# Performance work log

Measured on AMD Instinct MI355X. Metric: run time of the kernel, lower is better.

The kernel has to match this reference:

```python
import jax, jax.numpy as jnp
import numpy as np

FREQ_CUTOFF = 10.0
SAMPLING_RATE = 100.0
FILTER_TYPE = 'lowpass'

B, C, L = 64, 128, 8192


def setup_inputs() -> dict:
    key = jax.random.key(0)
    x = jax.random.normal(key, (B, C, L), dtype=jnp.float32)
    return {"x": x}


def reference(x):
    # x: [B, C, L]
    seq_len = x.shape[-1]
    x_fft = jnp.fft.fft(x, axis=-1)  # complex64 [B, C, L]
    freqs = jnp.fft.fftfreq(seq_len, 1.0 / SAMPLING_RATE)  # [L]
    if FILTER_TYPE == 'lowpass':
        mask = jnp.abs(freqs) < FREQ_CUTOFF
    elif FILTER_TYPE == 'highpass':
        mask = jnp.abs(freqs) > FREQ_CUTOFF
    else:
        raise ValueError('Invalid filter type: {}'.format(FILTER_TYPE))
    # Zero out masked frequency bins (faithful to original: lowpass zeroes |f| < cutoff)
    x_fft = jnp.where(mask[None, None, :], 0.0 + 0.0j, x_fft)
    x_filtered = jnp.real(jnp.fft.ifft(x_fft, axis=-1)).astype(jnp.float32)
    return x_filtered
```

## Files before the change

kernel.cpp:

```cpp
#include <hip/hip_runtime.h>
#include <hip/hip_fp16.h>


#define FFT_N 8192
#define NT    256
#define PHY(i) ((i) + ((i) >> 6))

typedef float v2f __attribute__((ext_vector_type(2)));
typedef float v4f __attribute__((ext_vector_type(4)));

__device__ __forceinline__ v2f cmul(v2f a, v2f b){
  v2f t, d;
  asm("v_pk_mul_f32 %0, %1, %2 op_sel:[0,0] op_sel_hi:[0,1]"
      : "=&v"(t) : "v"(a), "v"(b));
  asm("v_pk_fma_f32 %0, %1, %2, %3 op_sel:[1,1,0] op_sel_hi:[1,0,1] neg_lo:[0,1,0]"
      : "=v"(d) : "v"(a), "v"(b), "v"(t));
  return d;
}

__device__ __forceinline__ v2f mul_w32(v2f d, int j, bool cj){
  if (j == 0) return d;
  if (j == 8) return cj ? (v2f){-d.y, d.x} : (v2f){d.y, -d.x};
  const float C[16] = {1.f, 0.98078528f, 0.92387953f, 0.83146961f, 0.70710678f,
                       0.55557023f, 0.38268343f, 0.19509032f, 0.f, -0.19509032f,
                       -0.38268343f, -0.55557023f, -0.70710678f, -0.83146961f,
                       -0.92387953f, -0.98078528f};
  const float S[16] = {0.f, -0.19509032f, -0.38268343f, -0.55557023f, -0.70710678f,
                       -0.83146961f, -0.92387953f, -0.98078528f, -1.f, -0.98078528f,
                       -0.92387953f, -0.83146961f, -0.70710678f, -0.55557023f,
                       -0.38268343f, -0.19509032f};
  v2f w = {C[j], cj ? -S[j] : S[j]};
  return cmul(d, w);
}

template<int SZ, int L>
__device__ __forceinline__ void dif_rec(v2f* r){
  #pragma unroll
  for (int g = 0; g < SZ; g += 2*L){
    #pragma unroll
    for (int j = 0; j < L; ++j){
      v2f u = r[g+j], v = r[g+j+L];
      r[g+j]   = u + v;
      r[g+j+L] = mul_w32(u - v, j*(16/L), false);
    }
  }
  if constexpr (L > 1) dif_rec<SZ, L/2>(r);
}

template<int SZ, int L>
__device__ __forceinline__ void dit_rec(v2f* r){
  #pragma unroll
  for (int g = 0; g < SZ; g += 2*L){
    #pragma unroll
    for (int j = 0; j < L; ++j){
      v2f a = r[g+j];
      v2f b = mul_w32(r[g+j+L], j*(16/L), true);
      r[g+j]   = a + b;
      r[g+j+L] = a - b;
    }
  }
  if constexpr (2*L < SZ) dit_rec<SZ, 2*L>(r);
}

__host__ __device__ constexpr int brev5(int k){
  return ((k&1)<<4) | ((k&2)<<2) | (k&4) | ((k&8)>>2) | ((k&16)>>4);
}

__device__ __forceinline__ void twiddle_scale(v2f* r, int cbase, bool cj){
  float s, c;
  __sincosf((float)cbase * -7.6699039394282061e-4f, &s, &c);
  if (cj) s = -s;
  const v2f w1 = {c, s};
  v2f w2q = cmul(w1, w1);
  v2f w4q = cmul(w2q, w2q);
  v2f w8q = cmul(w4q, w4q);
  v2f w16 = cmul(w8q, w8q);
  v2f wa = w1;
  r[brev5(1)]  = cmul(r[brev5(1)],  wa);
  r[brev5(17)] = cmul(r[brev5(17)], cmul(w16, wa));
  #pragma unroll
  for (int k = 2; k <= 15; ++k){
    wa = cmul(wa, w1);
    r[brev5(k)]    = cmul(r[brev5(k)],    wa);
    r[brev5(k+16)] = cmul(r[brev5(k+16)], cmul(w16, wa));
  }
  r[brev5(16)] = cmul(r[brev5(16)], w16);
}

__device__ __forceinline__ void tw8(v2f* r, v2f w1){
  v2f w2 = cmul(w1, w1);
  v2f w3 = cmul(w2, w1);
  v2f w4 = cmul(w2, w2);
  v2f w5 = cmul(w4, w1);
  v2f w6 = cmul(w4, w2);
  v2f w7 = cmul(w4, w3);
  r[4] = cmul(r[4], w1);
  r[2] = cmul(r[2], w2);
  r[6] = cmul(r[6], w3);
  r[1] = cmul(r[1], w4);
  r[5] = cmul(r[5], w5);
  r[3] = cmul(r[3], w6);
  r[7] = cmul(r[7], w7);
}

__global__ __launch_bounds__(NT, 2)
void fourier_filter_kernel(const float* __restrict__ x, float* __restrict__ out){
  __shared__ __half2 zs[FFT_N + FFT_N/64];
  const int t = threadIdx.x;
  const long long pair = blockIdx.x;
  const float* r0 = x + pair * (2LL * FFT_N);
  const float* r1 = r0 + FFT_N;
  v2f r[32];

  const v2f W1C = {0.9999997058629f, -7.669903187e-4f};
  const v2f W2C = {0.9999988234517f, -1.5339801863e-3f};

  #pragma unroll
  for (int m = 0; m < 8; ++m){
    const int n = 4*t + (m << 10);
    const v4f a = *reinterpret_cast<const v4f*>(r0 + n);
    const v4f b = *reinterpret_cast<const v4f*>(r1 + n);
    r[0*8+m] = (v2f){a.x, b.x};
    r[1*8+m] = (v2f){a.y, b.y};
    r[2*8+m] = (v2f){a.z, b.z};
    r[3*8+m] = (v2f){a.w, b.w};
  }
  #pragma unroll
  for (int e = 0; e < 4; ++e) dif_rec<8, 4>(r + 8*e);
  {
    float s, c;
    __sincosf((float)(4*t) * -7.6699039394282061e-4f, &s, &c);
    v2f w0 = {c, s};
    v2f wA = cmul(w0, W1C);
    v2f wB = cmul(w0, W2C);
    v2f wC = cmul(wA, W2C);
    tw8(r + 0,  w0);
    tw8(r + 8,  wA);
    tw8(r + 16, wB);
    tw8(r + 24, wC);
  }
  #pragma unroll
  for (int e = 0; e < 4; ++e)
    #pragma unroll
    for (int m = 0; m < 8; ++m)
      zs[PHY(4*t + e + (m<<10))] = __floats2half2_rn(r[8*e+m].x, r[8*e+m].y);
  __syncthreads();

  const int base2 = ((t >> 5) << 10) | (t & 31);
  #pragma unroll
  for (int m = 0; m < 32; ++m){
    float2 f = __half22float2(zs[PHY(base2 + (m<<5))]);
    r[m] = (v2f){f.x, f.y};
  }
  dif_rec<32, 16>(r);
  twiddle_scale(r, (t & 31) << 3, false);
  #pragma unroll
  for (int m = 0; m < 32; ++m)
    zs[PHY(base2 + (m<<5))] = __floats2half2_rn(r[m].x, r[m].y);
  __syncthreads();

  #pragma unroll
  for (int e = 0; e < 32; ++e){
    float2 f = __half22float2(zs[PHY((t<<5) + e)]);
    r[e] = (v2f){f.x, f.y};
  }
  dif_rec<32, 16>(r);
  #pragma unroll
  for (int e = 0; e < 32; ++e){
    const int v  = (t << 5) + e;
    const int k  = (int)(__brev((unsigned)v) >> 19);
    const int kf = min(k, FFT_N - k);
    if (kf <= 819) r[e] = (v2f){0.f, 0.f};
  }
  dit_rec<32, 1>(r);
  #pragma unroll
  for (int e = 0; e < 32; ++e)
    zs[PHY((t<<5) + e)] = __floats2half2_rn(r[e].x, r[e].y);
  __syncthreads();

  #pragma unroll
  for (int m = 0; m < 32; ++m){
    float2 f = __half22float2(zs[PHY(base2 + (m<<5))]);
    r[m] = (v2f){f.x, f.y};
  }
  twiddle_scale(r, (t & 31) << 3, true);
  dit_rec<32, 1>(r);
  #pragma unroll
  for (int m = 0; m < 32; ++m)
    zs[PHY(base2 + (m<<5))] = __floats2half2_rn(r[m].x, r[m].y);
  __syncthreads();

  #pragma unroll
  for (int e = 0; e < 4; ++e)
    #pragma unroll
    for (int m = 0; m < 8; ++m){
      float2 f = __half22float2(zs[PHY(4*t + e + (m<<10))]);
      r[8*e+m] = (v2f){f.x, f.y};
    }
  {
    float s, c;
    __sincosf((float)(4*t) * -7.6699039394282061e-4f, &s, &c);
    v2f w0 = {c, -s};
    const v2f W1Cc = {W1C.x, -W1C.y};
    const v2f W2Cc = {W2C.x, -W2C.y};
    v2f wA = cmul(w0, W1Cc);
    v2f wB = cmul(w0, W2Cc);
    v2f wC = cmul(wA, W2Cc);
    tw8(r + 0,  w0);
    tw8(r + 8,  wA);
    tw8(r + 16, wB);
    tw8(r + 24, wC);
  }
  #pragma unroll
  for (int e = 0; e < 4; ++e) dit_rec<8, 1>(r + 8*e);

  const float invn = 1.f / (float)FFT_N;
  float* o0 = out + pair * (2LL * FFT_N);
  float* o1 = o0 + FFT_N;
  #pragma unroll
  for (int m = 0; m < 8; ++m){
    const int n = 4*t + (m << 10);
    v4f a, b;
    a.x = r[0*8+m].x * invn;  b.x = r[0*8+m].y * invn;
    a.y = r[1*8+m].x * invn;  b.y = r[1*8+m].y * invn;
    a.z = r[2*8+m].x * invn;  b.z = r[2*8+m].y * invn;
    a.w = r[3*8+m].x * invn;  b.w = r[3*8+m].y * invn;
    __builtin_nontemporal_store(a, reinterpret_cast<v4f*>(o0 + n));
    __builtin_nontemporal_store(b, reinterpret_cast<v4f*>(o1 + n));
  }
}

extern "C" void kernel_launch(void* const* d_in, const int* in_sizes, int n_in,
                              void* d_out, int out_size, void* d_ws, size_t ws_size,
                              hipStream_t stream) {
  const float* x = (const float*)d_in[0];
  float* out = (float*)d_out;
  const int total  = in_sizes[0];
  const int npairs = total / (2 * FFT_N);
  hipLaunchKernelGGL(fourier_filter_kernel, dim3(npairs), dim3(NT), 0, stream,
                     x, out);
}
```

Before: 104.3 us.

## Use persistent grid-stride blocks with register prefetch of next pair

The kernel becomes persistent: a fixed grid of 1024 blocks loops over row pairs with a grid stride. The next pair's input is loaded into registers before the current FFT work starts, so global load latency overlaps compute. This adds 64 registers of prefetch per thread and a trailing barrier per iteration, which may raise register pressure or cut occupancy under the 2-block launch bound.

Result: slower. 118.9 us (+14.0%).

```diff
diff --git a/kernel.cpp b/kernel.cpp
--- a/kernel.cpp
+++ b/kernel.cpp
@@ -4,6 +4,7 @@
 
 #define FFT_N 8192
 #define NT    256
+#define GRID  1024
 #define PHY(i) ((i) + ((i) >> 6))
 
 typedef float v2f __attribute__((ext_vector_type(2)));
@@ -104,129 +105,153 @@
 }
 
 __global__ __launch_bounds__(NT, 2)
-void fourier_filter_kernel(const float* __restrict__ x, float* __restrict__ out){
+void fourier_filter_kernel(const float* __restrict__ x, float* __restrict__ out,
+                           int npairs){
   __shared__ __half2 zs[FFT_N + FFT_N/64];
   const int t = threadIdx.x;
-  const long long pair = blockIdx.x;
-  const float* r0 = x + pair * (2LL * FFT_N);
-  const float* r1 = r0 + FFT_N;
-  v2f r[32];
 
   const v2f W1C = {0.9999997058629f, -7.669903187e-4f};
   const v2f W2C = {0.9999988234517f, -1.5339801863e-3f};
 
-  #pragma unroll
-  for (int m = 0; m < 8; ++m){
-    const int n = 4*t + (m << 10);
-    const v4f a = *reinterpret_cast<const v4f*>(r0 + n);
-    const v4f b = *reinterpret_cast<const v4f*>(r1 + n);
-    r[0*8+m] = (v2f){a.x, b.x};
-    r[1*8+m] = (v2f){a.y, b.y};
-    r[2*8+m] = (v2f){a.z, b.z};
-    r[3*8+m] = (v2f){a.w, b.w};
-  }
-  #pragma unroll
-  for (int e = 0; e < 4; ++e) dif_rec<8, 4>(r + 8*e);
+  v4f pfa[8], pfb[8];
+  long long pair = blockIdx.x;
   {
-    float s, c;
-    __sincosf((float)(4*t) * -7.6699039394282061e-4f, &s, &c);
-    v2f w0 = {c, s};
-    v2f wA = cmul(w0, W1C);
-    v2f wB = cmul(w0, W2C);
-    v2f wC = cmul(wA, W2C);
-    tw8(r + 0,  w0);
-    tw8(r + 8,  wA);
-    tw8(r + 16, wB);
-    tw8(r + 24, wC);
-  }
-  #pragma unroll
-  for (int e = 0; e < 4; ++e)
-    #pragma unroll
-    for (int m = 0; m < 8; ++m)
-      zs[PHY(4*t + e + (m<<10))] = __floats2half2_rn(r[8*e+m].x, r[8*e+m].y);
-  __syncthreads();
-
-  const int base2 = ((t >> 5) << 10) | (t & 31);
-  #pragma unroll
-  for (int m = 0; m < 32; ++m){
-    float2 f = __half22float2(zs[PHY(base2 + (m<<5))]);
-    r[m] = (v2f){f.x, f.y};
-  }
-  dif_rec<32, 16>(r);
-  twiddle_scale(r, (t & 31) << 3, false);
-  #pragma unroll
-  for (int m = 0; m < 32; ++m)
-    zs[PHY(base2 + (m<<5))] = __floats2half2_rn(r[m].x, r[m].y);
-  __syncthreads();
-
-  #pragma unroll
-  for (int e = 0; e < 32; ++e){
-    float2 f = __half22float2(zs[PHY((t<<5) + e)]);
-    r[e] = (v2f){f.x, f.y};
-  }
-  dif_rec<32, 16>(r);
-  #pragma unroll
-  for (int e = 0; e < 32; ++e){
-    const int v  = (t << 5) + e;
-    const int k  = (int)(__brev((unsigned)v) >> 19);
-    const int kf = min(k, FFT_N - k);
-    if (kf <= 819) r[e] = (v2f){0.f, 0.f};
-  }
-  dit_rec<32, 1>(r);
-  #pragma unroll
-  for (int e = 0; e < 32; ++e)
-    zs[PHY((t<<5) + e)] = __floats2half2_rn(r[e].x, r[e].y);
-  __syncthreads();
-
-  #pragma unroll
-  for (int m = 0; m < 32; ++m){
-    float2 f = __half22float2(zs[PHY(base2 + (m<<5))]);
-    r[m] = (v2f){f.x, f.y};
-  }
-  twiddle_scale(r, (t & 31) << 3, true);
-  dit_rec<32, 1>(r);
-  #pragma unroll
-  for (int m = 0; m < 32; ++m)
-    zs[PHY(base2 + (m<<5))] = __floats2half2_rn(r[m].x, r[m].y);
-  __syncthreads();
-
-  #pragma unroll
-  for (int e = 0; e < 4; ++e)
+    const float* q0 = x + pair * (2LL * FFT_N);
+    const float* q1 = q0 + FFT_N;
     #pragma unroll
     for (int m = 0; m < 8; ++m){
-      float2 f = __half22float2(zs[PHY(4*t + e + (m<<10))]);
-      r[8*e+m] = (v2f){f.x, f.y};
-    }
-  {
-    float s, c;
-    __sincosf((float)(4*t) * -7.6699039394282061e-4f, &s, &c);
-    v2f w0 = {c, -s};
-    const v2f W1Cc = {W1C.x, -W1C.y};
-    const v2f W2Cc = {W2C.x, -W2C.y};
-    v2f wA = cmul(w0, W1Cc);
-    v2f wB = cmul(w0, W2Cc);
-    v2f wC = cmul(wA, W2Cc);
-    tw8(r + 0,  w0);
-    tw8(r + 8,  wA);
-    tw8(r + 16, wB);
-    tw8(r + 24, wC);
-  }
-  #pragma unroll
-  for (int e = 0; e < 4; ++e) dit_rec<8, 1>(r + 8*e);
-
-  const float invn = 1.f / (float)FFT_N;
-  float* o0 = out + pair * (2LL * FFT_N);
-  float* o1 = o0 + FFT_N;
-  #pragma unroll
-  for (int m = 0; m < 8; ++m){
-    const int n = 4*t + (m << 10);
-    v4f a, b;
-    a.x = r[0*8+m].x * invn;  b.x = r[0*8+m].y * invn;
-    a.y = r[1*8+m].x * invn;  b.y = r[1*8+m].y * invn;
-    a.z = r[2*8+m].x * invn;  b.z = r[2*8+m].y * invn;
-    a.w = r[3*8+m].x * invn;  b.w = r[3*8+m].y * invn;
-    __builtin_nontemporal_store(a, reinterpret_cast<v4f*>(o0 + n));
-    __builtin_nontemporal_store(b, reinterpret_cast<v4f*>(o1 + n));
+      const int n = 4*t + (m << 10);
+      pfa[m] = *reinterpret_cast<const v4f*>(q0 + n);
+      pfb[m] = *reinterpret_cast<const v4f*>(q1 + n);
+    }
+  }
+
+  #pragma unroll 1
+  for (; pair < npairs; pair += GRID){
+    v2f r[32];
+
+    #pragma unroll
+    for (int m = 0; m < 8; ++m){
+      r[0*8+m] = (v2f){pfa[m].x, pfb[m].x};
+      r[1*8+m] = (v2f){pfa[m].y, pfb[m].y};
+      r[2*8+m] = (v2f){pfa[m].z, pfb[m].z};
+      r[3*8+m] = (v2f){pfa[m].w, pfb[m].w};
+    }
+    if (pair + GRID < npairs){
+      const float* q0 = x + (pair + GRID) * (2LL * FFT_N);
+      const float* q1 = q0 + FFT_N;
+      #pragma unroll
+      for (int m = 0; m < 8; ++m){
+        const int n = 4*t + (m << 10);
+        pfa[m] = *reinterpret_cast<const v4f*>(q0 + n);
+        pfb[m] = *reinterpret_cast<const v4f*>(q1 + n);
+      }
+    }
+
+    #pragma unroll
+    for (int e = 0; e < 4; ++e) dif_rec<8, 4>(r + 8*e);
+    {
+      float s, c;
+      __sincosf((float)(4*t) * -7.6699039394282061e-4f, &s, &c);
+      v2f w0 = {c, s};
+      v2f wA = cmul(w0, W1C);
+      v2f wB = cmul(w0, W2C);
+      v2f wC = cmul(wA, W2C);
+      tw8(r + 0,  w0);
+      tw8(r + 8,  wA);
+      tw8(r + 16, wB);
+      tw8(r + 24, wC);
+    }
+    #pragma unroll
+    for (int e = 0; e < 4; ++e)
+      #pragma unroll
+      for (int m = 0; m < 8; ++m)
+        zs[PHY(4*t + e + (m<<10))] = __floats2half2_rn(r[8*e+m].x, r[8*e+m].y);
+    __syncthreads();
+
+    const int base2 = ((t >> 5) << 10) | (t & 31);
+    #pragma unroll
+    for (int m = 0; m < 32; ++m){
+      float2 f = __half22float2(zs[PHY(base2 + (m<<5))]);
+      r[m] = (v2f){f.x, f.y};
+    }
+    dif_rec<32, 16>(r);
+    twiddle_scale(r, (t & 31) << 3, false);
+    #pragma unroll
+    for (int m = 0; m < 32; ++m)
+      zs[PHY(base2 + (m<<5))] = __floats2half2_rn(r[m].x, r[m].y);
+    __syncthreads();
+
+    #pragma unroll
+    for (int e = 0; e < 32; ++e){
+      float2 f = __half22float2(zs[PHY((t<<5) + e)]);
+      r[e] = (v2f){f.x, f.y};
+    }
+    dif_rec<32, 16>(r);
+    #pragma unroll
+    for (int e = 0; e < 32; ++e){
+      const int v  = (t << 5) + e;
+      const int k  = (int)(__brev((unsigned)v) >> 19);
+      const int kf = min(k, FFT_N - k);
+      if (kf <= 819) r[e] = (v2f){0.f, 0.f};
+    }
+    dit_rec<32, 1>(r);
+    #pragma unroll
+    for (int e = 0; e < 32; ++e)
+      zs[PHY((t<<5) + e)] = __floats2half2_rn(r[e].x, r[e].y);
+    __syncthreads();
+
+    #pragma unroll
+    for (int m = 0; m < 32; ++m){
+      float2 f = __half22float2(zs[PHY(base2 + (m<<5))]);
+      r[m] = (v2f){f.x, f.y};
+    }
+    twiddle_scale(r, (t & 31) << 3, true);
+    dit_rec<32, 1>(r);
+    #pragma unroll
+    for (int m = 0; m < 32; ++m)
+      zs[PHY(base2 + (m<<5))] = __floats2half2_rn(r[m].x, r[m].y);
+    __syncthreads();
+
+    #pragma unroll
+    for (int e = 0; e < 4; ++e)
+      #pragma unroll
+      for (int m = 0; m < 8; ++m){
+        float2 f = __half22float2(zs[PHY(4*t + e + (m<<10))]);
+        r[8*e+m] = (v2f){f.x, f.y};
+      }
+    {
+      float s, c;
+      __sincosf((float)(4*t) * -7.6699039394282061e-4f, &s, &c);
+      v2f w0 = {c, -s};
+      const v2f W1Cc = {W1C.x, -W1C.y};
+      const v2f W2Cc = {W2C.x, -W2C.y};
+      v2f wA = cmul(w0, W1Cc);
+      v2f wB = cmul(w0, W2Cc);
+      v2f wC = cmul(wA, W2Cc);
+      tw8(r + 0,  w0);
+      tw8(r + 8,  wA);
+      tw8(r + 16, wB);
+      tw8(r + 24, wC);
+    }
+    #pragma unroll
+    for (int e = 0; e < 4; ++e) dit_rec<8, 1>(r + 8*e);
+
+    const float invn = 1.f / (float)FFT_N;
+    float* o0 = out + pair * (2LL * FFT_N);
+    float* o1 = o0 + FFT_N;
+    #pragma unroll
+    for (int m = 0; m < 8; ++m){
+      const int n = 4*t + (m << 10);
+      v4f a, b;
+      a.x = r[0*8+m].x * invn;  b.x = r[0*8+m].y * invn;
+      a.y = r[1*8+m].x * invn;  b.y = r[1*8+m].y * invn;
+      a.z = r[2*8+m].x * invn;  b.z = r[2*8+m].y * invn;
+      a.w = r[3*8+m].x * invn;  b.w = r[3*8+m].y * invn;
+      __builtin_nontemporal_store(a, reinterpret_cast<v4f*>(o0 + n));
+      __builtin_nontemporal_store(b, reinterpret_cast<v4f*>(o1 + n));
+    }
+    __syncthreads();
   }
 }
 
@@ -237,6 +262,7 @@
   float* out = (float*)d_out;
   const int total  = in_sizes[0];
   const int npairs = total / (2 * FFT_N);
-  hipLaunchKernelGGL(fourier_filter_kernel, dim3(npairs), dim3(NT), 0, stream,
-                     x, out);
-}
+  const int grid   = npairs < GRID ? npairs : GRID;
+  hipLaunchKernelGGL(fourier_filter_kernel, dim3(grid), dim3(NT), 0, stream,
+                     x, out, npairs);
+}
```
